# Performance work log

Hardware: AMD Instinct MI355X
Metric: run time of the kernel (lower is better)

The kernel has to match this reference:

```python
import jax, jax.numpy as jnp
import numpy as np
from math import ceil


def _cubic(x, scale):
    # MATLAB-style antialiased cubic (Keys a=-0.5), scale <= 1
    x = np.asarray(x, dtype=np.float64) * scale
    ax = np.abs(x)
    ax2 = ax * ax
    ax3 = ax2 * ax
    w = (1.5 * ax3 - 2.5 * ax2 + 1.0) * (ax <= 1) + \
        (-0.5 * ax3 + 2.5 * ax2 - 4.0 * ax + 2.0) * ((ax > 1) & (ax <= 2))
    return w * scale


def _make_kernel(in_len, out_len):
    # Mirrors kernel() in the source: returns (taps[L], (pad_l, pad_r), stride).
    assert in_len >= out_len and in_len % out_len == 0
    scale = float(out_len) / float(in_len)
    klen = 4.0 / scale
    x = np.array([1, out_len], dtype=np.float64)
    u = x / scale + 0.5 * (1.0 - 1.0 / scale)
    left = np.floor(u - klen / 2.0)
    p = int(ceil(klen)) + 2
    ind = left[:, None] + np.arange(p) - 1
    indices = ind.astype(np.int64)
    weights = _cubic(u[:, None] - indices - 1, scale)
    weights = weights / weights.sum(axis=1, keepdims=True)
    keep = np.nonzero(np.any(weights, axis=0))[0]
    weights = weights[:, keep]
    indices = indices[:, keep]
    assert np.all(weights[0] == weights[-1])  # shift-invariant for integer stride
    pad_l = int(np.where(indices[0] == 0)[0][0])
    pad_r = indices.shape[1] - 1 - int(np.where(indices[-1] == in_len - 1)[0][0])
    return weights[0].astype(np.float32), (pad_l, pad_r), in_len // out_len


def setup_inputs() -> dict:
    key = jax.random.key(0)
    k1, k2 = jax.random.split(key)
    B, C, h, H = 32, 3, 128, 512
    inp = jax.random.uniform(k1, (B, C, h, h), dtype=jnp.float32)
    out = jax.random.uniform(k2, (B, C, H, H), dtype=jnp.float32)
    return {"input": inp, "output": out}


def reference(input, output):
    B, C, h, w = input.shape
    H, W = output.shape[2], output.shape[3]
    kh, ph, sh = _make_kernel(H, h)
    kw, pw, sw = _make_kernel(W, w)
    L = kh.shape[0]

    x = output.reshape(B * C, 1, H, W)  # depthwise via flattened channels
    # vertical pass: symmetric pad rows, conv with [L,1] kernel, stride (sh,1)
    x = jnp.pad(x, ((0, 0), (0, 0), (ph[0], ph[1]), (0, 0)), mode="symmetric")
    x = jax.lax.conv_general_dilated(
        x, jnp.asarray(kh).reshape(1, 1, L, 1), window_strides=(sh, 1),
        padding="VALID")
    # horizontal pass: symmetric pad cols, conv with [1,L] kernel, stride (1,sw)
    x = jnp.pad(x, ((0, 0), (0, 0), (0, 0), (pw[0], pw[1])), mode="symmetric")
    x = jax.lax.conv_general_dilated(
        x, jnp.asarray(kw).reshape(1, 1, 1, L), window_strides=(1, sw),
        padding="VALID")

    output_down = x.reshape(B, C, h, w)
    return jnp.mean(jnp.abs(output_down - input))
```

## Files before the change

### kernel.cpp

```cpp
#include <hip/hip_runtime.h>
#include <math.h>

#define BCN   96
#define IN_H  512
#define IN_W  512
#define OUT_H 128
#define OUT_W 128
#define TAPS  16
#define PAD   6
#define STRIDE 4
#define TR    8
#define IR    ((TR - 1) * STRIDE + TAPS)
#define NCH   (IR / 4)
#define NBLK  (BCN * (OUT_H / TR))
#define TOTAL_ELEMS (BCN * OUT_H * OUT_W)

struct K16 { float w[TAPS]; };

__device__ __forceinline__ int sym_idx(int i, int n) {
    i = (i < 0) ? (-1 - i) : i;
    return (i >= n) ? (2 * n - 1 - i) : i;
}

__device__ __forceinline__ int swz(int b) { return b ^ (((b >> 7) & 1) << 4); }

__global__ __launch_bounds__(256)
void bploss_kernel(const float* __restrict__ input,
                   const float* __restrict__ outimg,
                   float* __restrict__ loss, K16 kwa)
{
    __shared__ float dbuf[2][4 * IN_W];
    __shared__ float hrow[4][OUT_W];
    __shared__ float kwl[TAPS];
    __shared__ float wsum[4];

    const int tid  = threadIdx.x;
    const int bc   = blockIdx.x >> 4;
    const int tile = blockIdx.x & 15;
    const int r0   = tile * TR;
    const int iy0  = r0 * STRIDE - PAD;

    const float* img = outimg + (size_t)bc * IN_H * IN_W;

    auto gsrc = [&](int ch, int s) -> const float4* {
        const int y = sym_idx(iy0 + ch * 4 + (s >> 7), IN_H);
        return reinterpret_cast<const float4*>(img + (size_t)y * IN_W + (s & 127) * 4);
    };
    auto lslot = [&](float* buf, int s) -> float4* {
        return reinterpret_cast<float4*>(reinterpret_cast<char*>(buf) + swz(s << 4));
    };

    {
        float4 a = *gsrc(0, tid);
        float4 b = *gsrc(0, tid + 256);
        *lslot(dbuf[0], tid)       = a;
        *lslot(dbuf[0], tid + 256) = b;
    }
    if (tid < TAPS) kwl[tid] = kwa.w[tid];
    __syncthreads();

    const int pr = tid >> 6;
    const int c  = tid & 63;
    const int vb = tid >> 7;
    const int vx = tid & 127;

    int f0 = 8 * c - 8;
    f0 = (f0 < 0) ? 0 : f0;
    f0 = (f0 > 488) ? 488 : f0;
    const int Lbase = pr * (IN_W * 4) + f0 * 4;

    float vacc[4] = {0.f, 0.f, 0.f, 0.f};

    for (int ch = 0; ch < NCH; ++ch) {
        const int chn = (ch + 1 < NCH) ? (ch + 1) : (NCH - 1);
        const float4 n0 = *gsrc(chn, tid);
        const float4 n1 = *gsrc(chn, tid + 256);

        const char* raw = reinterpret_cast<const char*>(dbuf[ch & 1]);
        const float4 w0 = *reinterpret_cast<const float4*>(raw + swz(Lbase));
        const float4 w1 = *reinterpret_cast<const float4*>(raw + swz(Lbase + 16));
        const float4 w2 = *reinterpret_cast<const float4*>(raw + swz(Lbase + 32));
        const float4 w3 = *reinterpret_cast<const float4*>(raw + swz(Lbase + 48));
        const float4 w4 = *reinterpret_cast<const float4*>(raw + swz(Lbase + 64));
        const float4 w5 = *reinterpret_cast<const float4*>(raw + swz(Lbase + 80));
        const float win[24] = { w0.x,w0.y,w0.z,w0.w, w1.x,w1.y,w1.z,w1.w,
                                w2.x,w2.y,w2.z,w2.w, w3.x,w3.y,w3.z,w3.w,
                                w4.x,w4.y,w4.z,w4.w, w5.x,w5.y,w5.z,w5.w };
        float acc0 = 0.f, acc1 = 0.f;
        #pragma unroll
        for (int t = 0; t < TAPS; ++t) {
            acc0 += kwa.w[t] * win[t + 2];
            acc1 += kwa.w[t] * win[t + 6];
        }
        if (c == 0) {
            float a0 = 0.f, a1 = 0.f;
            #pragma unroll
            for (int t = 0; t < TAPS; ++t) {
                const int i0 = (t < 6) ? (5 - t) : (t - 6);
                const int i1 = (t < 2) ? (1 - t) : (t - 2);
                a0 += kwa.w[t] * win[i0];
                a1 += kwa.w[t] * win[i1];
            }
            acc0 = a0; acc1 = a1;
        } else if (c == 63) {
            float a0 = 0.f, a1 = 0.f;
            #pragma unroll
            for (int t = 0; t < TAPS; ++t) {
                const int i0 = (t <= 13) ? (10 + t) : ((t == 14) ? 23 : 22);
                const int i1 = (t <= 9) ? (14 + t) : (33 - t);
                a0 += kwa.w[t] * win[i0];
                a1 += kwa.w[t] * win[i1];
            }
            acc0 = a0; acc1 = a1;
        }
        *reinterpret_cast<float2*>(&hrow[pr][2 * c]) = make_float2(acc0, acc1);

        __syncthreads();

        const float h0 = hrow[0][vx], h1 = hrow[1][vx],
                    h2 = hrow[2][vx], h3 = hrow[3][vx];
        #pragma unroll
        for (int k = 0; k < 4; ++k) {
            const int t0 = 4 * (ch - (4 * vb + k));
            if (t0 >= 0 && t0 < TAPS) {
                vacc[k] += kwl[t0] * h0 + kwl[t0 + 1] * h1
                         + kwl[t0 + 2] * h2 + kwl[t0 + 3] * h3;
            }
        }

        *lslot(dbuf[(ch + 1) & 1], tid)       = n0;
        *lslot(dbuf[(ch + 1) & 1], tid + 256) = n1;
        __syncthreads();
    }

    float lsum = 0.f;
    #pragma unroll
    for (int k = 0; k < 4; ++k) {
        const int yo = r0 + 4 * vb + k;
        const float ref = input[((size_t)bc * OUT_H + yo) * OUT_W + vx];
        lsum += fabsf(vacc[k] - ref);
    }

    #pragma unroll
    for (int off = 32; off > 0; off >>= 1)
        lsum += __shfl_down(lsum, off, 64);

    const int wid = tid >> 6, lane = tid & 63;
    if (lane == 0) wsum[wid] = lsum;
    __syncthreads();
    if (tid == 0) {
        const float s = wsum[0] + wsum[1] + wsum[2] + wsum[3];
        atomicAdd(loss, s * (1.0f / (float)TOTAL_ELEMS));
    }
}

static void make_weights(K16* kw) {
    const double scale = 0.25;
    double w[TAPS]; double s = 0.0;
    for (int t = 0; t < TAPS; ++t) {
        const double ax = fabs((7.5 - (double)t) * scale);
        double v;
        if (ax <= 1.0)      v = 1.5 * ax * ax * ax - 2.5 * ax * ax + 1.0;
        else if (ax <= 2.0) v = -0.5 * ax * ax * ax + 2.5 * ax * ax - 4.0 * ax + 2.0;
        else                v = 0.0;
        w[t] = v * scale; s += w[t];
    }
    for (int t = 0; t < TAPS; ++t) kw->w[t] = (float)(w[t] / s);
}

extern "C" void kernel_launch(void* const* d_in, const int* in_sizes, int n_in,
                              void* d_out, int out_size, void* d_ws, size_t ws_size,
                              hipStream_t stream) {
    const float* input;
    const float* outimg;
    if (in_sizes[0] == TOTAL_ELEMS) {
        input  = (const float*)d_in[0];
        outimg = (const float*)d_in[1];
    } else {
        input  = (const float*)d_in[1];
        outimg = (const float*)d_in[0];
    }
    float* loss = (float*)d_out;

    K16 kw;
    make_weights(&kw);

    hipMemsetAsync(d_out, 0, sizeof(float), stream);
    bploss_kernel<<<NBLK, 256, 0, stream>>>(input, outimg, loss, kw);
}
```

Measured before the change: 170.5 us.

## Split fused separable conv into horizontal and vertical kernels via workspace

Replaces the single fused kernel with two kernels. The first computes the horizontal 16-tap strided convolution for every input row and writes a 512x128 intermediate per image to workspace. The second applies the vertical convolution, takes the L1 difference against the reference and reduces it. The aim is to remove the per-block halo re-reads and the barrier-heavy chunk loop of the fused version, at the cost of an extra global round trip of about 25MB and a second launch. The fused kernel remains as a fallback when the workspace is too small.

```diff
diff --git a/kernel.cpp b/kernel.cpp
--- a/kernel.cpp
+++ b/kernel.cpp
@@ -9,25 +9,134 @@
 #define TAPS  16
 #define PAD   6
 #define STRIDE 4
+#define TOTAL_ELEMS (BCN * OUT_H * OUT_W)
+#define INTER_BYTES ((size_t)BCN * IN_H * OUT_W * 4)
+
+struct K16 { float w[TAPS]; };
+
+__device__ __forceinline__ int sym_idx(int i, int n) {
+    i = (i < 0) ? (-1 - i) : i;
+    return (i >= n) ? (2 * n - 1 - i) : i;
+}
+
+__device__ __forceinline__ int swz(int b) { return b ^ (((b >> 7) & 7) << 4); }
+
+__global__ __launch_bounds__(256)
+void hconv_kernel(const float* __restrict__ outimg,
+                  float* __restrict__ inter,
+                  K16 kwa)
+{
+    __shared__ float rowbuf[4][IN_W];
+    const int tid = threadIdx.x;
+    const int w   = tid >> 6;
+    const int c   = tid & 63;
+    const int gr  = blockIdx.x * 4 + w;
+    const int bc  = gr >> 9;
+    const int y   = gr & 511;
+    const float* row = outimg + ((size_t)bc * IN_H + y) * IN_W;
+
+    char* lbase = reinterpret_cast<char*>(rowbuf[w]);
+    {
+        const float4 a = reinterpret_cast<const float4*>(row)[c];
+        const float4 b = reinterpret_cast<const float4*>(row)[c + 64];
+        *reinterpret_cast<float4*>(lbase + swz(16 * c))        = a;
+        *reinterpret_cast<float4*>(lbase + swz(1024 + 16 * c)) = b;
+    }
+    asm volatile("s_waitcnt lgkmcnt(0)" ::: "memory");
+
+    int f0 = 8 * c - 8;
+    f0 = (f0 < 0) ? 0 : (f0 > 488 ? 488 : f0);
+    const int B0 = 4 * f0;
+    const float4 w0 = *reinterpret_cast<const float4*>(lbase + swz(B0));
+    const float4 w1 = *reinterpret_cast<const float4*>(lbase + swz(B0 + 16));
+    const float4 w2 = *reinterpret_cast<const float4*>(lbase + swz(B0 + 32));
+    const float4 w3 = *reinterpret_cast<const float4*>(lbase + swz(B0 + 48));
+    const float4 w4 = *reinterpret_cast<const float4*>(lbase + swz(B0 + 64));
+    const float4 w5 = *reinterpret_cast<const float4*>(lbase + swz(B0 + 80));
+    const float win[24] = { w0.x,w0.y,w0.z,w0.w, w1.x,w1.y,w1.z,w1.w,
+                            w2.x,w2.y,w2.z,w2.w, w3.x,w3.y,w3.z,w3.w,
+                            w4.x,w4.y,w4.z,w4.w, w5.x,w5.y,w5.z,w5.w };
+    float acc0 = 0.f, acc1 = 0.f;
+    #pragma unroll
+    for (int t = 0; t < TAPS; ++t) {
+        acc0 += kwa.w[t] * win[t + 2];
+        acc1 += kwa.w[t] * win[t + 6];
+    }
+    if (c == 0) {
+        float a0 = 0.f, a1 = 0.f;
+        #pragma unroll
+        for (int t = 0; t < TAPS; ++t) {
+            const int i0 = (t < 6) ? (5 - t) : (t - 6);
+            const int i1 = (t < 2) ? (1 - t) : (t - 2);
+            a0 += kwa.w[t] * win[i0];
+            a1 += kwa.w[t] * win[i1];
+        }
+        acc0 = a0; acc1 = a1;
+    } else if (c == 63) {
+        float a0 = 0.f, a1 = 0.f;
+        #pragma unroll
+        for (int t = 0; t < TAPS; ++t) {
+            const int i0 = (t <= 13) ? (10 + t) : ((t == 14) ? 23 : 22);
+            const int i1 = (t <= 9) ? (14 + t) : (33 - t);
+            a0 += kwa.w[t] * win[i0];
+            a1 += kwa.w[t] * win[i1];
+        }
+        acc0 = a0; acc1 = a1;
+    }
+    reinterpret_cast<float2*>(inter + ((size_t)bc * IN_H + y) * OUT_W)[c] =
+        make_float2(acc0, acc1);
+}
+
+__global__ __launch_bounds__(256)
+void vconv_kernel(const float* __restrict__ inter,
+                  const float* __restrict__ input,
+                  float* __restrict__ loss, K16 kwa)
+{
+    __shared__ float wsum[4];
+    const int tid = threadIdx.x;
+    const int bc  = blockIdx.x >> 5;
+    const int rq  = blockIdx.x & 31;
+    const int c   = tid & 63;
+    const int yl  = tid >> 6;
+    const int yo  = rq * 4 + yl;
+    const float* src = inter + (size_t)bc * IN_H * OUT_W;
+
+    float a0 = 0.f, a1 = 0.f;
+    const int ybase = STRIDE * yo - PAD;
+    #pragma unroll
+    for (int t = 0; t < TAPS; ++t) {
+        const int r = sym_idx(ybase + t, IN_H);
+        const float2 v = reinterpret_cast<const float2*>(src + (size_t)r * OUT_W)[c];
+        a0 += kwa.w[t] * v.x;
+        a1 += kwa.w[t] * v.y;
+    }
+    const float2 ref =
+        reinterpret_cast<const float2*>(input + ((size_t)bc * OUT_H + yo) * OUT_W)[c];
+    float lsum = fabsf(a0 - ref.x) + fabsf(a1 - ref.y);
+
+    #pragma unroll
+    for (int off = 32; off > 0; off >>= 1)
+        lsum += __shfl_down(lsum, off, 64);
+    const int wid = tid >> 6, lane = tid & 63;
+    if (lane == 0) wsum[wid] = lsum;
+    __syncthreads();
+    if (tid == 0) {
+        const float s = wsum[0] + wsum[1] + wsum[2] + wsum[3];
+        atomicAdd(loss, s * (1.0f / (float)TOTAL_ELEMS));
+    }
+}
+
 #define TR    8
 #define IR    ((TR - 1) * STRIDE + TAPS)
 #define NCH   (IR / 4)
 #define NBLK  (BCN * (OUT_H / TR))
-#define TOTAL_ELEMS (BCN * OUT_H * OUT_W)
-
-struct K16 { float w[TAPS]; };
-
-__device__ __forceinline__ int sym_idx(int i, int n) {
-    i = (i < 0) ? (-1 - i) : i;
-    return (i >= n) ? (2 * n - 1 - i) : i;
-}
-
-__device__ __forceinline__ int swz(int b) { return b ^ (((b >> 7) & 1) << 4); }
+
+__device__ __forceinline__ int swz1(int b) { return b ^ (((b >> 7) & 1) << 4); }
 
 __global__ __launch_bounds__(256)
-void bploss_kernel(const float* __restrict__ input,
-                   const float* __restrict__ outimg,
-                   float* __restrict__ loss, K16 kwa)
+void bploss_fallback(const float* __restrict__ input,
+                     const float* __restrict__ outimg,
+                     float* __restrict__ loss, K16 kwa)
 {
     __shared__ float dbuf[2][4 * IN_W];
     __shared__ float hrow[4][OUT_W];
@@ -39,7 +148,6 @@
     const int tile = blockIdx.x & 15;
     const int r0   = tile * TR;
     const int iy0  = r0 * STRIDE - PAD;
-
     const float* img = outimg + (size_t)bc * IN_H * IN_W;
 
     auto gsrc = [&](int ch, int s) -> const float4* {
@@ -47,9 +155,8 @@
         return reinterpret_cast<const float4*>(img + (size_t)y * IN_W + (s & 127) * 4);
     };
     auto lslot = [&](float* buf, int s) -> float4* {
-        return reinterpret_cast<float4*>(reinterpret_cast<char*>(buf) + swz(s << 4));
+        return reinterpret_cast<float4*>(reinterpret_cast<char*>(buf) + swz1(s << 4));
     };
-
     {
         float4 a = *gsrc(0, tid);
         float4 b = *gsrc(0, tid + 256);
@@ -63,26 +170,22 @@
     const int c  = tid & 63;
     const int vb = tid >> 7;
     const int vx = tid & 127;
-
     int f0 = 8 * c - 8;
-    f0 = (f0 < 0) ? 0 : f0;
-    f0 = (f0 > 488) ? 488 : f0;
+    f0 = (f0 < 0) ? 0 : (f0 > 488 ? 488 : f0);
     const int Lbase = pr * (IN_W * 4) + f0 * 4;
-
     float vacc[4] = {0.f, 0.f, 0.f, 0.f};
 
     for (int ch = 0; ch < NCH; ++ch) {
         const int chn = (ch + 1 < NCH) ? (ch + 1) : (NCH - 1);
         const float4 n0 = *gsrc(chn, tid);
         const float4 n1 = *gsrc(chn, tid + 256);
-
         const char* raw = reinterpret_cast<const char*>(dbuf[ch & 1]);
-        const float4 w0 = *reinterpret_cast<const float4*>(raw + swz(Lbase));
-        const float4 w1 = *reinterpret_cast<const float4*>(raw + swz(Lbase + 16));
-        const float4 w2 = *reinterpret_cast<const float4*>(raw + swz(Lbase + 32));
-        const float4 w3 = *reinterpret_cast<const float4*>(raw + swz(Lbase + 48));
-        const float4 w4 = *reinterpret_cast<const float4*>(raw + swz(Lbase + 64));
-        const float4 w5 = *reinterpret_cast<const float4*>(raw + swz(Lbase + 80));
+        const float4 w0 = *reinterpret_cast<const float4*>(raw + swz1(Lbase));
+        const float4 w1 = *reinterpret_cast<const float4*>(raw + swz1(Lbase + 16));
+        const float4 w2 = *reinterpret_cast<const float4*>(raw + swz1(Lbase + 32));
+        const float4 w3 = *reinterpret_cast<const float4*>(raw + swz1(Lbase + 48));
+        const float4 w4 = *reinterpret_cast<const float4*>(raw + swz1(Lbase + 64));
+        const float4 w5 = *reinterpret_cast<const float4*>(raw + swz1(Lbase + 80));
         const float win[24] = { w0.x,w0.y,w0.z,w0.w, w1.x,w1.y,w1.z,w1.w,
                                 w2.x,w2.y,w2.z,w2.w, w3.x,w3.y,w3.z,w3.w,
                                 w4.x,w4.y,w4.z,w4.w, w5.x,w5.y,w5.z,w5.w };
@@ -114,9 +217,7 @@
             acc0 = a0; acc1 = a1;
         }
         *reinterpret_cast<float2*>(&hrow[pr][2 * c]) = make_float2(acc0, acc1);
-
         __syncthreads();
-
         const float h0 = hrow[0][vx], h1 = hrow[1][vx],
                     h2 = hrow[2][vx], h3 = hrow[3][vx];
         #pragma unroll
@@ -127,7 +228,6 @@
                          + kwl[t0 + 2] * h2 + kwl[t0 + 3] * h3;
             }
         }
-
         *lslot(dbuf[(ch + 1) & 1], tid)       = n0;
         *lslot(dbuf[(ch + 1) & 1], tid + 256) = n1;
         __syncthreads();
@@ -140,11 +240,9 @@
         const float ref = input[((size_t)bc * OUT_H + yo) * OUT_W + vx];
         lsum += fabsf(vacc[k] - ref);
     }
-
     #pragma unroll
     for (int off = 32; off > 0; off >>= 1)
         lsum += __shfl_down(lsum, off, 64);
-
     const int wid = tid >> 6, lane = tid & 63;
     if (lane == 0) wsum[wid] = lsum;
     __syncthreads();
@@ -186,5 +284,11 @@
     make_weights(&kw);
 
     hipMemsetAsync(d_out, 0, sizeof(float), stream);
-    bploss_kernel<<<NBLK, 256, 0, stream>>>(input, outimg, loss, kw);
-}
+    if (ws_size >= INTER_BYTES) {
+        float* inter = (float*)d_ws;
+        hconv_kernel<<<BCN * IN_H / 4, 256, 0, stream>>>(outimg, inter, kw);
+        vconv_kernel<<<BCN * (OUT_H / 4), 256, 0, stream>>>(inter, input, loss, kw);
+    } else {
+        bploss_fallback<<<NBLK, 256, 0, stream>>>(input, outimg, loss, kw);
+    }
+}
```

Result: slower. 192.7 us (+13.0%).

## Deepen global prefetch to three chunks and use one barrier per iteration

Applied to the files above, without the earlier changes.

Global loads are now issued three chunks ahead into a four-slot register ring instead of one chunk ahead. The hrow staging buffer is double-buffered so the next LDS tile can be written before the barrier, which drops one of the two __syncthreads per iteration in favor of a manual lgkmcnt wait plus s_barrier. The loop is fully unrolled. This is meant to hide memory latency and cut synchronization cost, at the price of more registers from the ring and unrolling.

```diff
diff --git a/kernel.cpp b/kernel.cpp
--- a/kernel.cpp
+++ b/kernel.cpp
@@ -22,7 +22,7 @@
     return (i >= n) ? (2 * n - 1 - i) : i;
 }
 
-__device__ __forceinline__ int swz(int b) { return b ^ (((b >> 7) & 1) << 4); }
+__device__ __forceinline__ int swz1(int b) { return b ^ (((b >> 7) & 1) << 4); }
 
 __global__ __launch_bounds__(256)
 void bploss_kernel(const float* __restrict__ input,
@@ -30,7 +30,7 @@
                    float* __restrict__ loss, K16 kwa)
 {
     __shared__ float dbuf[2][4 * IN_W];
-    __shared__ float hrow[4][OUT_W];
+    __shared__ float hrow[2][4][OUT_W];
     __shared__ float kwl[TAPS];
     __shared__ float wsum[4];
 
@@ -39,7 +39,6 @@
     const int tile = blockIdx.x & 15;
     const int r0   = tile * TR;
     const int iy0  = r0 * STRIDE - PAD;
-
     const float* img = outimg + (size_t)bc * IN_H * IN_W;
 
     auto gsrc = [&](int ch, int s) -> const float4* {
@@ -47,42 +46,46 @@
         return reinterpret_cast<const float4*>(img + (size_t)y * IN_W + (s & 127) * 4);
     };
     auto lslot = [&](float* buf, int s) -> float4* {
-        return reinterpret_cast<float4*>(reinterpret_cast<char*>(buf) + swz(s << 4));
+        return reinterpret_cast<float4*>(reinterpret_cast<char*>(buf) + swz1(s << 4));
     };
 
-    {
-        float4 a = *gsrc(0, tid);
-        float4 b = *gsrc(0, tid + 256);
-        *lslot(dbuf[0], tid)       = a;
-        *lslot(dbuf[0], tid + 256) = b;
+    if (tid < TAPS) kwl[tid] = kwa.w[tid];
+
+    float4 rA[4], rB[4];
+    #pragma unroll
+    for (int c0 = 0; c0 < 3; ++c0) {
+        rA[c0] = *gsrc(c0, tid);
+        rB[c0] = *gsrc(c0, tid + 256);
     }
-    if (tid < TAPS) kwl[tid] = kwa.w[tid];
-    __syncthreads();
+    *lslot(dbuf[0], tid)       = rA[0];
+    *lslot(dbuf[0], tid + 256) = rB[0];
+    asm volatile("s_waitcnt lgkmcnt(0)" ::: "memory");
+    __builtin_amdgcn_s_barrier();
+    __builtin_amdgcn_sched_barrier(0);
 
     const int pr = tid >> 6;
     const int c  = tid & 63;
     const int vb = tid >> 7;
     const int vx = tid & 127;
-
     int f0 = 8 * c - 8;
-    f0 = (f0 < 0) ? 0 : f0;
-    f0 = (f0 > 488) ? 488 : f0;
+    f0 = (f0 < 0) ? 0 : (f0 > 488 ? 488 : f0);
     const int Lbase = pr * (IN_W * 4) + f0 * 4;
-
     float vacc[4] = {0.f, 0.f, 0.f, 0.f};
 
-    for (int ch = 0; ch < NCH; ++ch) {
-        const int chn = (ch + 1 < NCH) ? (ch + 1) : (NCH - 1);
-        const float4 n0 = *gsrc(chn, tid);
-        const float4 n1 = *gsrc(chn, tid + 256);
+    #pragma unroll
+    for (int i = 0; i < NCH; ++i) {
+        if (i + 3 < NCH) {
+            rA[(i + 3) & 3] = *gsrc(i + 3, tid);
+            rB[(i + 3) & 3] = *gsrc(i + 3, tid + 256);
+        }
 
-        const char* raw = reinterpret_cast<const char*>(dbuf[ch & 1]);
-        const float4 w0 = *reinterpret_cast<const float4*>(raw + swz(Lbase));
-        const float4 w1 = *reinterpret_cast<const float4*>(raw + swz(Lbase + 16));
-        const float4 w2 = *reinterpret_cast<const float4*>(raw + swz(Lbase + 32));
-        const float4 w3 = *reinterpret_cast<const float4*>(raw + swz(Lbase + 48));
-        const float4 w4 = *reinterpret_cast<const float4*>(raw + swz(Lbase + 64));
-        const float4 w5 = *reinterpret_cast<const float4*>(raw + swz(Lbase + 80));
+        const char* raw = reinterpret_cast<const char*>(dbuf[i & 1]);
+        const float4 w0 = *reinterpret_cast<const float4*>(raw + swz1(Lbase));
+        const float4 w1 = *reinterpret_cast<const float4*>(raw + swz1(Lbase + 16));
+        const float4 w2 = *reinterpret_cast<const float4*>(raw + swz1(Lbase + 32));
+        const float4 w3 = *reinterpret_cast<const float4*>(raw + swz1(Lbase + 48));
+        const float4 w4 = *reinterpret_cast<const float4*>(raw + swz1(Lbase + 64));
+        const float4 w5 = *reinterpret_cast<const float4*>(raw + swz1(Lbase + 80));
         const float win[24] = { w0.x,w0.y,w0.z,w0.w, w1.x,w1.y,w1.z,w1.w,
                                 w2.x,w2.y,w2.z,w2.w, w3.x,w3.y,w3.z,w3.w,
                                 w4.x,w4.y,w4.z,w4.w, w5.x,w5.y,w5.z,w5.w };
@@ -113,24 +116,27 @@
             }
             acc0 = a0; acc1 = a1;
         }
-        *reinterpret_cast<float2*>(&hrow[pr][2 * c]) = make_float2(acc0, acc1);
+        *reinterpret_cast<float2*>(&hrow[i & 1][pr][2 * c]) = make_float2(acc0, acc1);
 
-        __syncthreads();
+        if (i + 1 < NCH) {
+            *lslot(dbuf[(i + 1) & 1], tid)       = rA[(i + 1) & 3];
+            *lslot(dbuf[(i + 1) & 1], tid + 256) = rB[(i + 1) & 3];
+        }
 
-        const float h0 = hrow[0][vx], h1 = hrow[1][vx],
-                    h2 = hrow[2][vx], h3 = hrow[3][vx];
+        asm volatile("s_waitcnt lgkmcnt(0)" ::: "memory");
+        __builtin_amdgcn_s_barrier();
+        __builtin_amdgcn_sched_barrier(0);
+
+        const float h0 = hrow[i & 1][0][vx], h1 = hrow[i & 1][1][vx],
+                    h2 = hrow[i & 1][2][vx], h3 = hrow[i & 1][3][vx];
         #pragma unroll
         for (int k = 0; k < 4; ++k) {
-            const int t0 = 4 * (ch - (4 * vb + k));
+            const int t0 = 4 * (i - (4 * vb + k));
             if (t0 >= 0 && t0 < TAPS) {
                 vacc[k] += kwl[t0] * h0 + kwl[t0 + 1] * h1
                          + kwl[t0 + 2] * h2 + kwl[t0 + 3] * h3;
             }
         }
-
-        *lslot(dbuf[(ch + 1) & 1], tid)       = n0;
-        *lslot(dbuf[(ch + 1) & 1], tid + 256) = n1;
-        __syncthreads();
     }
 
     float lsum = 0.f;
@@ -140,11 +146,9 @@
         const float ref = input[((size_t)bc * OUT_H + yo) * OUT_W + vx];
         lsum += fabsf(vacc[k] - ref);
     }
-
     #pragma unroll
     for (int off = 32; off > 0; off >>= 1)
         lsum += __shfl_down(lsum, off, 64);
-
     const int wid = tid >> 6, lane = tid & 63;
     if (lane == 0) wsum[wid] = lsum;
     __syncthreads();
```

Result: no change. 169.2 us (-0.8%).
